# Kernel tuning notes

Measured on AMD Instinct MI355X. Metric: run time of the kernel, lower is better.

Reference implementation:

```python
import jax, jax.numpy as jnp
import numpy as np

N_NODES = 100000
N_EDGES = 3200000
D_IN = 128
D_HID = 128
D_FF = 256
N_CLASSES = 26
N_GRAPHS = 512


def setup_inputs() -> dict:
    key = jax.random.key(0)
    ks = jax.random.split(key, 12)
    s = 0.05
    return {
        "x": jax.random.normal(ks[0], (N_NODES, D_IN), dtype=jnp.float32),
        "edge_index": jax.random.randint(ks[1], (2, N_EDGES), 0, N_NODES, dtype=jnp.int64),
        "batch": jnp.sort(jax.random.randint(ks[2], (N_NODES,), 0, N_GRAPHS, dtype=jnp.int64)),
        "W1": jax.random.normal(ks[3], (D_IN, D_HID), dtype=jnp.float32) * s,
        "b1": jnp.zeros((D_HID,), dtype=jnp.float32),
        "W2": jax.random.normal(ks[4], (D_HID, D_HID), dtype=jnp.float32) * s,
        "b2": jnp.zeros((D_HID,), dtype=jnp.float32),
        "W3": jax.random.normal(ks[5], (D_HID, D_HID), dtype=jnp.float32) * s,
        "b3": jnp.zeros((D_HID,), dtype=jnp.float32),
        "Wfc": jax.random.normal(ks[6], (D_HID, D_FF), dtype=jnp.float32) * s,
        "bfc": jnp.zeros((D_FF,), dtype=jnp.float32),
        "Wfc2": jax.random.normal(ks[7], (D_FF, N_CLASSES), dtype=jnp.float32) * s,
        "bfc2": jnp.zeros((N_CLASSES,), dtype=jnp.float32),
    }


def _gcn_layer(x, src, dst, norm, W, b):
    # GCNConv: h = x @ W; out[dst] += norm_e * h[src]; out += b
    h = x @ W                                   # [N, D]
    msg = h[src] * norm[:, None]                # [E+N, D] gather + scale
    agg = jax.ops.segment_sum(msg, dst, num_segments=N_NODES)
    return agg + b


def reference(x, edge_index, batch, W1, b1, W2, b2, W3, b3, Wfc, bfc, Wfc2, bfc2):
    # add self-loops (PyG GCNConv default) and compute symmetric normalization once
    loop = jnp.arange(N_NODES, dtype=edge_index.dtype)
    src = jnp.concatenate([edge_index[0], loop])
    dst = jnp.concatenate([edge_index[1], loop])
    deg = jax.ops.segment_sum(jnp.ones_like(dst, dtype=x.dtype), dst, num_segments=N_NODES)
    dinv = jnp.where(deg > 0, jax.lax.rsqrt(deg), 0.0)
    norm = dinv[src] * dinv[dst]               # D^{-1/2} A_hat D^{-1/2}

    h = jax.nn.relu(_gcn_layer(x, src, dst, norm, W1, b1))
    h = jax.nn.relu(_gcn_layer(h, src, dst, norm, W2, b2))
    h = jax.nn.relu(_gcn_layer(h, src, dst, norm, W3, b3))

    # global mean pool over graphs
    sums = jax.ops.segment_sum(h, batch, num_segments=N_GRAPHS)       # [G, D]
    cnts = jax.ops.segment_sum(jnp.ones((h.shape[0],), h.dtype), batch, num_segments=N_GRAPHS)
    pooled = sums / jnp.maximum(cnts, 1.0)[:, None]

    out = jax.nn.relu(pooled @ Wfc + bfc)       # dropout is identity at inference
    return out @ Wfc2 + bfc2                    # [G, num_classes]
```

## Files before the change

### kernel.cpp

```cpp
#include <hip/hip_runtime.h>
#include <hip/hip_bf16.h>

typedef __bf16 bf16;
typedef __attribute__((ext_vector_type(8))) __bf16 bf16x8;
typedef __attribute__((ext_vector_type(4))) __bf16 bf16x4;
typedef __attribute__((ext_vector_type(2))) __bf16 bf16x2;
typedef __attribute__((ext_vector_type(4))) float f32x4;

constexpr int N_NODES   = 100000;
constexpr int N_PAD     = 100032;
constexpr int D         = 128;
constexpr int D_FF      = 256;
constexpr int N_CLASSES = 26;
constexpr int N_GRAPHS  = 512;
constexpr int NB1       = 1024;
constexpr int NBUCK     = (N_NODES + 511) / 512;

__device__ inline float2 bf2f(unsigned u) {
    float lo = __uint_as_float(u << 16);
    float hi = __uint_as_float(u & 0xffff0000u);
    return make_float2(lo, hi);
}


__global__ __launch_bounds__(256) void p1_hist(const int* __restrict__ edst,
                                               int* __restrict__ gcount, int e) {
    __shared__ int cnt[NBUCK];
    for (int t = threadIdx.x; t < NBUCK; t += 256) cnt[t] = 0;
    __syncthreads();
    int chunk = (e + NB1 - 1) / NB1;
    int lo = blockIdx.x * chunk;
    int hi = min(e, lo + chunk);
    for (int i = lo + threadIdx.x; i < hi; i += 256)
        atomicAdd(&cnt[edst[i] >> 9], 1);
    __syncthreads();
    for (int t = threadIdx.x; t < NBUCK; t += 256)
        gcount[t * NB1 + blockIdx.x] = cnt[t];
}

__global__ __launch_bounds__(256) void scan1(const int* __restrict__ in,
                                             int* out, int* bsum, int n) {
    __shared__ int sd[256];
    int i = blockIdx.x * 256 + threadIdx.x;
    int v = (i < n) ? in[i] : 0;
    sd[threadIdx.x] = v; __syncthreads();
    for (int off = 1; off < 256; off <<= 1) {
        int t = (threadIdx.x >= off) ? sd[threadIdx.x - off] : 0;
        __syncthreads();
        sd[threadIdx.x] += t;
        __syncthreads();
    }
    if (i < n) out[i + 1] = sd[threadIdx.x];
    if (threadIdx.x == 255) bsum[blockIdx.x] = sd[255];
}

__global__ __launch_bounds__(1024) void scan2(const int* __restrict__ bsum,
                                              int* boff, int nb) {
    __shared__ int sd[1024];
    int t = threadIdx.x;
    int v = (t < nb) ? bsum[t] : 0;
    sd[t] = v; __syncthreads();
    for (int off = 1; off < 1024; off <<= 1) {
        int x = (t >= off) ? sd[t - off] : 0;
        __syncthreads();
        sd[t] += x;
        __syncthreads();
    }
    if (t < nb) boff[t] = sd[t] - v;
}

__global__ void scan3(int* out, const int* __restrict__ boff, int n) {
    int i = blockIdx.x * 256 + threadIdx.x;
    if (i < n) out[i + 1] += boff[blockIdx.x];
    if (i == 0) out[0] = 0;
}

__global__ __launch_bounds__(256) void p3_scatter(const int* __restrict__ esrc,
                                                  const int* __restrict__ edst,
                                                  const int* __restrict__ gbase,
                                                  int* __restrict__ ebuf, int e) {
    __shared__ int cur[NBUCK];
    for (int t = threadIdx.x; t < NBUCK; t += 256)
        cur[t] = gbase[t * NB1 + blockIdx.x];
    __syncthreads();
    int chunk = (e + NB1 - 1) / NB1;
    int lo = blockIdx.x * chunk;
    int hi = min(e, lo + chunk);
    for (int i = lo + threadIdx.x; i < hi; i += 256) {
        int d = edst[i], s = esrc[i];
        int pos = atomicAdd(&cur[d >> 9], 1);
        ebuf[pos] = (s << 9) | (d & 511);
    }
}

__global__ __launch_bounds__(256) void p45_fill(const int* __restrict__ ebuf,
                                                const int* __restrict__ gbase,
                                                float* __restrict__ dinv,
                                                int* __restrict__ rowptr,
                                                int* __restrict__ csrc, int e, int n) {
    __shared__ int cnt[512];
    __shared__ int ps[256];
    __shared__ int cur[512];
    int b = blockIdx.x, t = threadIdx.x;
    cnt[t] = 0; cnt[t + 256] = 0;
    __syncthreads();
    int lo = gbase[b * NB1];
    int hi = (b + 1 < NBUCK) ? gbase[(b + 1) * NB1] : e;
    for (int i = lo + t; i < hi; i += 256)
        atomicAdd(&cnt[ebuf[i] & 511], 1);
    __syncthreads();
    int a0 = cnt[t * 2], a1 = cnt[t * 2 + 1];
    ps[t] = a0 + a1;
    __syncthreads();
    for (int off = 1; off < 256; off <<= 1) {
        int v = (t >= off) ? ps[t - off] : 0;
        __syncthreads();
        ps[t] += v;
        __syncthreads();
    }
    int pexcl = (t > 0) ? ps[t - 1] : 0;
    int g0 = lo + pexcl;
    int node0 = b * 512 + t * 2;
    cur[t * 2] = g0;
    cur[t * 2 + 1] = g0 + a0;
    if (node0 < n) {
        rowptr[node0] = g0;
        dinv[node0] = 1.0f / sqrtf((float)(a0 + 1));
    }
    if (node0 + 1 < n) {
        rowptr[node0 + 1] = g0 + a0;
        dinv[node0 + 1] = 1.0f / sqrtf((float)(a1 + 1));
    }
    if (b == 0 && t == 0) rowptr[n] = e;
    __syncthreads();
    for (int i = lo + t; i < hi; i += 256) {
        int pe = ebuf[i];
        int pos = atomicAdd(&cur[pe & 511], 1);
        csrc[pos] = pe >> 9;
    }
}

__global__ __launch_bounds__(576) void starts_kernel(const int* __restrict__ batch,
                                                     int* __restrict__ starts, int n) {
    int g = threadIdx.x;
    if (g > N_GRAPHS) return;
    int lo = 0, hi = n;
    while (lo < hi) {
        int mid = (lo + hi) >> 1;
        if (batch[mid] < g) lo = mid + 1; else hi = mid;
    }
    starts[g] = lo;
}


__global__ void castWT3_kernel(const float* __restrict__ W0,
                               const float* __restrict__ W1,
                               const float* __restrict__ W2,
                               bf16* __restrict__ WT3) {
    int n = blockIdx.x, l = blockIdx.y, k = threadIdx.x;
    const float* W = (l == 0) ? W0 : (l == 1) ? W1 : W2;
    WT3[l * D * D + n * D + k] = (bf16)W[k * D + n];
}

__global__ __launch_bounds__(256) void gemm_kernel(const bf16* __restrict__ A,
                                                   const bf16* __restrict__ WT,
                                                   bf16* __restrict__ C) {
    int wave = threadIdx.x >> 6;
    int lane = threadIdx.x & 63;
    int m16  = lane & 15;
    int quad = lane >> 4;
    int row0 = blockIdx.x * 64 + wave * 16;

    bf16x8 a[4];
    const bf16* arow = A + (row0 + m16) * D + quad * 8;
#pragma unroll
    for (int kt = 0; kt < 4; ++kt)
        a[kt] = *(const bf16x8*)(arow + kt * 32);

#pragma unroll
    for (int nt = 0; nt < 8; ++nt) {
        f32x4 acc = {0.f, 0.f, 0.f, 0.f};
        const bf16* brow = WT + (nt * 16 + m16) * D + quad * 8;
#pragma unroll
        for (int kt = 0; kt < 4; ++kt) {
            bf16x8 b = *(const bf16x8*)(brow + kt * 32);
            acc = __builtin_amdgcn_mfma_f32_16x16x32_bf16(a[kt], b, acc, 0, 0, 0);
        }
#pragma unroll
        for (int r = 0; r < 4; ++r)
            C[(row0 + quad * 4 + r) * D + nt * 16 + m16] = (bf16)acc[r];
    }
}

__global__ __launch_bounds__(256) void gemm_f32_kernel(const float* __restrict__ A,
                                                       const bf16* __restrict__ WT,
                                                       bf16* __restrict__ C, int n) {
    int wave = threadIdx.x >> 6;
    int lane = threadIdx.x & 63;
    int m16  = lane & 15;
    int quad = lane >> 4;
    int row0 = blockIdx.x * 64 + wave * 16;
    int arowi = row0 + m16;

    bf16x8 a[4];
    const float* arow = A + (size_t)arowi * D + quad * 8;
#pragma unroll
    for (int kt = 0; kt < 4; ++kt) {
        float4 f0 = make_float4(0.f, 0.f, 0.f, 0.f);
        float4 f1 = make_float4(0.f, 0.f, 0.f, 0.f);
        if (arowi < n) {
            f0 = *(const float4*)(arow + kt * 32);
            f1 = *(const float4*)(arow + kt * 32 + 4);
        }
        bf16x8 v = { (bf16)f0.x, (bf16)f0.y, (bf16)f0.z, (bf16)f0.w,
                     (bf16)f1.x, (bf16)f1.y, (bf16)f1.z, (bf16)f1.w };
        a[kt] = v;
    }

#pragma unroll
    for (int nt = 0; nt < 8; ++nt) {
        f32x4 acc = {0.f, 0.f, 0.f, 0.f};
        const bf16* brow = WT + (nt * 16 + m16) * D + quad * 8;
#pragma unroll
        for (int kt = 0; kt < 4; ++kt) {
            bf16x8 b = *(const bf16x8*)(brow + kt * 32);
            acc = __builtin_amdgcn_mfma_f32_16x16x32_bf16(a[kt], b, acc, 0, 0, 0);
        }
#pragma unroll
        for (int r = 0; r < 4; ++r)
            C[(row0 + quad * 4 + r) * D + nt * 16 + m16] = (bf16)acc[r];
    }
}

__global__ __launch_bounds__(256) void spmm_kernel(const bf16* __restrict__ h,
                                                   const int* __restrict__ rowptr,
                                                   const int* __restrict__ csrc,
                                                   const float* __restrict__ dinv,
                                                   const float* __restrict__ bias,
                                                   bf16* __restrict__ out, int n) {
    int v = blockIdx.x * 4 + (threadIdx.x >> 6);
    if (v >= n) return;
    int lane = threadIdx.x & 63;
    int g = lane >> 4;
    int c = lane & 15;
    int s = rowptr[v], e = rowptr[v + 1];
    float dv = dinv[v];

    float acc[8] = {0.f, 0.f, 0.f, 0.f, 0.f, 0.f, 0.f, 0.f};

    if (g == 0) {
        uint4 u = *(const uint4*)(h + v * D + c * 8);
        float s2 = dv * dv;
        float2 f0 = bf2f(u.x), f1 = bf2f(u.y), f2 = bf2f(u.z), f3 = bf2f(u.w);
        acc[0] = s2 * f0.x; acc[1] = s2 * f0.y;
        acc[2] = s2 * f1.x; acc[3] = s2 * f1.y;
        acc[4] = s2 * f2.x; acc[5] = s2 * f2.y;
        acc[6] = s2 * f3.x; acc[7] = s2 * f3.y;
    }

    int j = s + g;
    for (; j + 4 < e; j += 8) {
        int s0 = csrc[j], s1 = csrc[j + 4];
        float w0 = dinv[s0] * dv, w1 = dinv[s1] * dv;
        uint4 ua = *(const uint4*)(h + s0 * D + c * 8);
        uint4 ub = *(const uint4*)(h + s1 * D + c * 8);
        float2 a0 = bf2f(ua.x), a1 = bf2f(ua.y), a2 = bf2f(ua.z), a3 = bf2f(ua.w);
        float2 b0 = bf2f(ub.x), b1 = bf2f(ub.y), b2 = bf2f(ub.z), b3 = bf2f(ub.w);
        acc[0] = fmaf(w0, a0.x, acc[0]); acc[1] = fmaf(w0, a0.y, acc[1]);
        acc[2] = fmaf(w0, a1.x, acc[2]); acc[3] = fmaf(w0, a1.y, acc[3]);
        acc[4] = fmaf(w0, a2.x, acc[4]); acc[5] = fmaf(w0, a2.y, acc[5]);
        acc[6] = fmaf(w0, a3.x, acc[6]); acc[7] = fmaf(w0, a3.y, acc[7]);
        acc[0] = fmaf(w1, b0.x, acc[0]); acc[1] = fmaf(w1, b0.y, acc[1]);
        acc[2] = fmaf(w1, b1.x, acc[2]); acc[3] = fmaf(w1, b1.y, acc[3]);
        acc[4] = fmaf(w1, b2.x, acc[4]); acc[5] = fmaf(w1, b2.y, acc[5]);
        acc[6] = fmaf(w1, b3.x, acc[6]); acc[7] = fmaf(w1, b3.y, acc[7]);
    }
    if (j < e) {
        int s0 = csrc[j];
        float w0 = dinv[s0] * dv;
        uint4 ua = *(const uint4*)(h + s0 * D + c * 8);
        float2 a0 = bf2f(ua.x), a1 = bf2f(ua.y), a2 = bf2f(ua.z), a3 = bf2f(ua.w);
        acc[0] = fmaf(w0, a0.x, acc[0]); acc[1] = fmaf(w0, a0.y, acc[1]);
        acc[2] = fmaf(w0, a1.x, acc[2]); acc[3] = fmaf(w0, a1.y, acc[3]);
        acc[4] = fmaf(w0, a2.x, acc[4]); acc[5] = fmaf(w0, a2.y, acc[5]);
        acc[6] = fmaf(w0, a3.x, acc[6]); acc[7] = fmaf(w0, a3.y, acc[7]);
    }

#pragma unroll
    for (int d = 0; d < 8; ++d) {
        acc[d] += __shfl_xor(acc[d], 16);
        acc[d] += __shfl_xor(acc[d], 32);
    }

    if (g == 0) {
        float4 bi0 = *(const float4*)(bias + c * 8);
        float4 bi1 = *(const float4*)(bias + c * 8 + 4);
        bf16x8 o;
        o[0] = (bf16)fmaxf(acc[0] + bi0.x, 0.f);
        o[1] = (bf16)fmaxf(acc[1] + bi0.y, 0.f);
        o[2] = (bf16)fmaxf(acc[2] + bi0.z, 0.f);
        o[3] = (bf16)fmaxf(acc[3] + bi0.w, 0.f);
        o[4] = (bf16)fmaxf(acc[4] + bi1.x, 0.f);
        o[5] = (bf16)fmaxf(acc[5] + bi1.y, 0.f);
        o[6] = (bf16)fmaxf(acc[6] + bi1.z, 0.f);
        o[7] = (bf16)fmaxf(acc[7] + bi1.w, 0.f);
        *(bf16x8*)(out + v * D + c * 8) = o;
    }
}

__global__ __launch_bounds__(256) void pool_kernel(const bf16* __restrict__ h,
                                                   const int* __restrict__ starts,
                                                   float* __restrict__ pooled) {
    __shared__ float part[3][D];
    int g = blockIdx.x;
    int w = threadIdx.x >> 6, lane = threadIdx.x & 63;
    int s = starts[g], e = starts[g + 1];
    float ax = 0.f, ay = 0.f;
    for (int r = s + w; r < e; r += 4) {
        unsigned u = *(const unsigned*)(h + r * D + lane * 2);
        float2 f = bf2f(u);
        ax += f.x; ay += f.y;
    }
    if (w > 0) { part[w - 1][lane * 2] = ax; part[w - 1][lane * 2 + 1] = ay; }
    __syncthreads();
    if (w == 0) {
#pragma unroll
        for (int k = 0; k < 3; ++k) { ax += part[k][lane * 2]; ay += part[k][lane * 2 + 1]; }
        float c = fmaxf((float)(e - s), 1.0f);
        pooled[g * D + lane * 2]     = ax / c;
        pooled[g * D + lane * 2 + 1] = ay / c;
    }
}

__global__ __launch_bounds__(256) void fc_kernel(const float* __restrict__ pooled,
                                                 const float* __restrict__ Wfc,
                                                 const float* __restrict__ bfc,
                                                 const float* __restrict__ Wfc2,
                                                 const float* __restrict__ bfc2,
                                                 float* __restrict__ out) {
    __shared__ float pr[D];
    __shared__ float hid[D_FF];
    int g = blockIdx.x, t = threadIdx.x;
    if (t < D) pr[t] = pooled[g * D + t];
    __syncthreads();
    float acc = bfc[t];
    for (int k = 0; k < D; ++k) acc = fmaf(pr[k], Wfc[k * D_FF + t], acc);
    hid[t] = fmaxf(acc, 0.f);
    __syncthreads();
    if (t < N_CLASSES) {
        float o = bfc2[t];
        for (int k = 0; k < D_FF; ++k) o = fmaf(hid[k], Wfc2[k * N_CLASSES + t], o);
        out[g * N_CLASSES + t] = o;
    }
}


extern "C" void kernel_launch(void* const* d_in, const int* in_sizes, int n_in,
                              void* d_out, int out_size, void* d_ws, size_t ws_size,
                              hipStream_t stream) {
    const float* x     = (const float*)d_in[0];
    const int*   eidx  = (const int*)d_in[1];
    const int*   batch = (const int*)d_in[2];
    const float* W[3]  = { (const float*)d_in[3], (const float*)d_in[5], (const float*)d_in[7] };
    const float* b[3]  = { (const float*)d_in[4], (const float*)d_in[6], (const float*)d_in[8] };
    const float* Wfc   = (const float*)d_in[9];
    const float* bfc   = (const float*)d_in[10];
    const float* Wfc2  = (const float*)d_in[11];
    const float* bfc2  = (const float*)d_in[12];
    float* out = (float*)d_out;

    const int E = in_sizes[1] / 2;
    const int N = in_sizes[0] / D;
    const int* esrc = eidx;
    const int* edst = eidx + E;

    uint8_t* base = (uint8_t*)d_ws;
    size_t off = 0;
    auto alloc = [&](size_t bytes) -> void* {
        void* p = base + off;
        off = (off + bytes + 255) & ~(size_t)255;
        return p;
    };
    bf16*  hA     = (bf16*) alloc((size_t)N_PAD * D * 2);
    bf16*  hB     = (bf16*) alloc((size_t)N_PAD * D * 2);
    bf16*  WT3    = (bf16*) alloc((size_t)3 * D * D * 2);
    int*   csrc   = (int*)  alloc((size_t)E * 4);
    int*   ebuf   = (int*)  alloc((size_t)E * 4);
    int*   gcount = (int*)  alloc((size_t)NBUCK * NB1 * 4);
    int*   gbase  = (int*)  alloc((size_t)(NBUCK * NB1 + 1) * 4);
    int*   rowptr = (int*)  alloc((size_t)(N + 1) * 4);
    float* dinv   = (float*)alloc((size_t)N * 4);
    int*   bsum   = (int*)  alloc(4096);
    int*   boff   = (int*)  alloc(4096);
    int*   starts = (int*)  alloc((size_t)(N_GRAPHS + 1) * 4);
    float* pooled = (float*)alloc((size_t)N_GRAPHS * D * 4);
    (void)ws_size; (void)n_in; (void)out_size;

    const int GB  = N_PAD / 64;
    const int SB  = (N + 3) / 4;
    const int GCN = NBUCK * NB1;
    const int GCB = (GCN + 255) / 256;

    p1_hist<<<NB1, 256, 0, stream>>>(edst, gcount, E);
    scan1<<<GCB, 256, 0, stream>>>(gcount, gbase, bsum, GCN);
    scan2<<<1, 1024, 0, stream>>>(bsum, boff, GCB);
    scan3<<<GCB, 256, 0, stream>>>(gbase, boff, GCN);
    p3_scatter<<<NB1, 256, 0, stream>>>(esrc, edst, gbase, ebuf, E);
    p45_fill<<<NBUCK, 256, 0, stream>>>(ebuf, gbase, dinv, rowptr, csrc, E, N);

    starts_kernel<<<1, 576, 0, stream>>>(batch, starts, N);

    castWT3_kernel<<<dim3(D, 3), D, 0, stream>>>(W[0], W[1], W[2], WT3);

    gemm_f32_kernel<<<GB, 256, 0, stream>>>(x, WT3, hA, N);
    spmm_kernel<<<SB, 256, 0, stream>>>(hA, rowptr, csrc, dinv, b[0], hB, N);
    for (int l = 1; l < 3; ++l) {
        gemm_kernel<<<GB, 256, 0, stream>>>(hB, WT3 + (size_t)l * D * D, hA);
        spmm_kernel<<<SB, 256, 0, stream>>>(hA, rowptr, csrc, dinv, b[l], hB, N);
    }

    pool_kernel<<<N_GRAPHS, 256, 0, stream>>>(hB, starts, pooled);
    fc_kernel<<<N_GRAPHS, 256, 0, stream>>>(pooled, Wfc, bfc, Wfc2, bfc2, out);
}
```

Baseline: 675.2 us.

## Fuse preprocessing kernels, single-block scan, and merge pooling with FC head

Merges the first-layer GEMM, the edge-destination histogram and the graph-start search into one multi-role prep kernel. The three-pass scan becomes a single-block scan, and the histogram block count drops from 1024 to 256. Scatter and fill kernels move to 512 threads, and pooling is fused with the MLP head. The aim is to cut kernel launches and shrink the scan. The cost is less parallelism in the histogram and scatter stages, plus a serial per-thread scan loop.

New measurement: 719.2 us. 1.07x slower.

```diff
diff --git a/kernel.cpp b/kernel.cpp
--- a/kernel.cpp
+++ b/kernel.cpp
@@ -3,8 +3,6 @@
 
 typedef __bf16 bf16;
 typedef __attribute__((ext_vector_type(8))) __bf16 bf16x8;
-typedef __attribute__((ext_vector_type(4))) __bf16 bf16x4;
-typedef __attribute__((ext_vector_type(2))) __bf16 bf16x2;
 typedef __attribute__((ext_vector_type(4))) float f32x4;
 
 constexpr int N_NODES   = 100000;
@@ -13,8 +11,10 @@
 constexpr int D_FF      = 256;
 constexpr int N_CLASSES = 26;
 constexpr int N_GRAPHS  = 512;
-constexpr int NB1       = 1024;
+constexpr int NB1       = 256;
 constexpr int NBUCK     = (N_NODES + 511) / 512;
+constexpr int GB        = N_PAD / 64;
+constexpr int GCN       = NBUCK * NB1;
 
 __device__ inline float2 bf2f(unsigned u) {
     float lo = __uint_as_float(u << 16);
@@ -22,136 +22,152 @@
     return make_float2(lo, hi);
 }
 
-
-__global__ __launch_bounds__(256) void p1_hist(const int* __restrict__ edst,
-                                               int* __restrict__ gcount, int e) {
+__global__ __launch_bounds__(256) void prep_kernel(const float* __restrict__ x,
+                                                   const bf16* __restrict__ WT,
+                                                   bf16* __restrict__ hA,
+                                                   const int* __restrict__ edst,
+                                                   int* __restrict__ gcount,
+                                                   const int* __restrict__ batch,
+                                                   int* __restrict__ starts,
+                                                   int e, int n) {
     __shared__ int cnt[NBUCK];
-    for (int t = threadIdx.x; t < NBUCK; t += 256) cnt[t] = 0;
-    __syncthreads();
-    int chunk = (e + NB1 - 1) / NB1;
-    int lo = blockIdx.x * chunk;
-    int hi = min(e, lo + chunk);
-    for (int i = lo + threadIdx.x; i < hi; i += 256)
-        atomicAdd(&cnt[edst[i] >> 9], 1);
-    __syncthreads();
-    for (int t = threadIdx.x; t < NBUCK; t += 256)
-        gcount[t * NB1 + blockIdx.x] = cnt[t];
-}
-
-__global__ __launch_bounds__(256) void scan1(const int* __restrict__ in,
-                                             int* out, int* bsum, int n) {
-    __shared__ int sd[256];
-    int i = blockIdx.x * 256 + threadIdx.x;
-    int v = (i < n) ? in[i] : 0;
-    sd[threadIdx.x] = v; __syncthreads();
-    for (int off = 1; off < 256; off <<= 1) {
-        int t = (threadIdx.x >= off) ? sd[threadIdx.x - off] : 0;
-        __syncthreads();
-        sd[threadIdx.x] += t;
-        __syncthreads();
-    }
-    if (i < n) out[i + 1] = sd[threadIdx.x];
-    if (threadIdx.x == 255) bsum[blockIdx.x] = sd[255];
-}
-
-__global__ __launch_bounds__(1024) void scan2(const int* __restrict__ bsum,
-                                              int* boff, int nb) {
+    int bx = blockIdx.x;
+    if (bx < GB) {
+        int wave = threadIdx.x >> 6;
+        int lane = threadIdx.x & 63;
+        int m16  = lane & 15;
+        int quad = lane >> 4;
+        int row0 = bx * 64 + wave * 16;
+        int arowi = row0 + m16;
+
+        bf16x8 a[4];
+        const float* arow = x + (size_t)arowi * D + quad * 8;
+#pragma unroll
+        for (int kt = 0; kt < 4; ++kt) {
+            float4 f0 = make_float4(0.f, 0.f, 0.f, 0.f);
+            float4 f1 = make_float4(0.f, 0.f, 0.f, 0.f);
+            if (arowi < n) {
+                f0 = *(const float4*)(arow + kt * 32);
+                f1 = *(const float4*)(arow + kt * 32 + 4);
+            }
+            bf16x8 v = { (bf16)f0.x, (bf16)f0.y, (bf16)f0.z, (bf16)f0.w,
+                         (bf16)f1.x, (bf16)f1.y, (bf16)f1.z, (bf16)f1.w };
+            a[kt] = v;
+        }
+#pragma unroll
+        for (int nt = 0; nt < 8; ++nt) {
+            f32x4 acc = {0.f, 0.f, 0.f, 0.f};
+            const bf16* brow = WT + (nt * 16 + m16) * D + quad * 8;
+#pragma unroll
+            for (int kt = 0; kt < 4; ++kt) {
+                bf16x8 b = *(const bf16x8*)(brow + kt * 32);
+                acc = __builtin_amdgcn_mfma_f32_16x16x32_bf16(a[kt], b, acc, 0, 0, 0);
+            }
+#pragma unroll
+            for (int r = 0; r < 4; ++r)
+                hA[(row0 + quad * 4 + r) * D + nt * 16 + m16] = (bf16)acc[r];
+        }
+    } else if (bx < GB + NB1) {
+        int b = bx - GB;
+        for (int t = threadIdx.x; t < NBUCK; t += 256) cnt[t] = 0;
+        __syncthreads();
+        int chunk = (e + NB1 - 1) / NB1;
+        int lo = b * chunk;
+        int hi = min(e, lo + chunk);
+        for (int i = lo + threadIdx.x; i < hi; i += 256)
+            atomicAdd(&cnt[edst[i] >> 9], 1);
+        __syncthreads();
+        for (int t = threadIdx.x; t < NBUCK; t += 256)
+            gcount[t * NB1 + b] = cnt[t];
+    } else {
+        for (int g = threadIdx.x; g <= N_GRAPHS; g += 256) {
+            int lo = 0, hi = n;
+            while (lo < hi) {
+                int mid = (lo + hi) >> 1;
+                if (batch[mid] < g) lo = mid + 1; else hi = mid;
+            }
+            starts[g] = lo;
+        }
+    }
+}
+
+__global__ __launch_bounds__(1024) void scan_single(const int* __restrict__ in,
+                                                    int* __restrict__ outx, int n) {
     __shared__ int sd[1024];
     int t = threadIdx.x;
-    int v = (t < nb) ? bsum[t] : 0;
-    sd[t] = v; __syncthreads();
+    const int CH = (n + 1023) / 1024;
+    int lo = t * CH, hi = min(n, lo + CH);
+    int sum = 0;
+    for (int i = lo; i < hi; ++i) sum += in[i];
+    sd[t] = sum; __syncthreads();
     for (int off = 1; off < 1024; off <<= 1) {
-        int x = (t >= off) ? sd[t - off] : 0;
-        __syncthreads();
-        sd[t] += x;
-        __syncthreads();
-    }
-    if (t < nb) boff[t] = sd[t] - v;
-}
-
-__global__ void scan3(int* out, const int* __restrict__ boff, int n) {
-    int i = blockIdx.x * 256 + threadIdx.x;
-    if (i < n) out[i + 1] += boff[blockIdx.x];
-    if (i == 0) out[0] = 0;
-}
-
-__global__ __launch_bounds__(256) void p3_scatter(const int* __restrict__ esrc,
+        int v = (t >= off) ? sd[t - off] : 0;
+        __syncthreads();
+        sd[t] += v;
+        __syncthreads();
+    }
+    int run = sd[t] - sum;
+    for (int i = lo; i < hi; ++i) { int v = in[i]; outx[i] = run; run += v; }
+}
+
+__global__ __launch_bounds__(512) void p3_scatter(const int* __restrict__ esrc,
                                                   const int* __restrict__ edst,
                                                   const int* __restrict__ gbase,
                                                   int* __restrict__ ebuf, int e) {
     __shared__ int cur[NBUCK];
-    for (int t = threadIdx.x; t < NBUCK; t += 256)
+    for (int t = threadIdx.x; t < NBUCK; t += 512)
         cur[t] = gbase[t * NB1 + blockIdx.x];
     __syncthreads();
     int chunk = (e + NB1 - 1) / NB1;
     int lo = blockIdx.x * chunk;
     int hi = min(e, lo + chunk);
-    for (int i = lo + threadIdx.x; i < hi; i += 256) {
+    for (int i = lo + threadIdx.x; i < hi; i += 512) {
         int d = edst[i], s = esrc[i];
         int pos = atomicAdd(&cur[d >> 9], 1);
         ebuf[pos] = (s << 9) | (d & 511);
     }
 }
 
-__global__ __launch_bounds__(256) void p45_fill(const int* __restrict__ ebuf,
+__global__ __launch_bounds__(512) void p45_fill(const int* __restrict__ ebuf,
                                                 const int* __restrict__ gbase,
                                                 float* __restrict__ dinv,
                                                 int* __restrict__ rowptr,
                                                 int* __restrict__ csrc, int e, int n) {
     __shared__ int cnt[512];
-    __shared__ int ps[256];
+    __shared__ int ps[512];
     __shared__ int cur[512];
     int b = blockIdx.x, t = threadIdx.x;
-    cnt[t] = 0; cnt[t + 256] = 0;
+    cnt[t] = 0;
     __syncthreads();
     int lo = gbase[b * NB1];
     int hi = (b + 1 < NBUCK) ? gbase[(b + 1) * NB1] : e;
-    for (int i = lo + t; i < hi; i += 256)
+    for (int i = lo + t; i < hi; i += 512)
         atomicAdd(&cnt[ebuf[i] & 511], 1);
     __syncthreads();
-    int a0 = cnt[t * 2], a1 = cnt[t * 2 + 1];
-    ps[t] = a0 + a1;
-    __syncthreads();
-    for (int off = 1; off < 256; off <<= 1) {
+    int a = cnt[t];
+    ps[t] = a;
+    __syncthreads();
+    for (int off = 1; off < 512; off <<= 1) {
         int v = (t >= off) ? ps[t - off] : 0;
         __syncthreads();
         ps[t] += v;
         __syncthreads();
     }
-    int pexcl = (t > 0) ? ps[t - 1] : 0;
-    int g0 = lo + pexcl;
-    int node0 = b * 512 + t * 2;
-    cur[t * 2] = g0;
-    cur[t * 2 + 1] = g0 + a0;
-    if (node0 < n) {
-        rowptr[node0] = g0;
-        dinv[node0] = 1.0f / sqrtf((float)(a0 + 1));
-    }
-    if (node0 + 1 < n) {
-        rowptr[node0 + 1] = g0 + a0;
-        dinv[node0 + 1] = 1.0f / sqrtf((float)(a1 + 1));
+    int g0 = lo + ps[t] - a;
+    int node = b * 512 + t;
+    cur[t] = g0;
+    if (node < n) {
+        rowptr[node] = g0;
+        dinv[node] = 1.0f / sqrtf((float)(a + 1));
     }
     if (b == 0 && t == 0) rowptr[n] = e;
     __syncthreads();
-    for (int i = lo + t; i < hi; i += 256) {
+    for (int i = lo + t; i < hi; i += 512) {
         int pe = ebuf[i];
         int pos = atomicAdd(&cur[pe & 511], 1);
         csrc[pos] = pe >> 9;
     }
 }
-
-__global__ __launch_bounds__(576) void starts_kernel(const int* __restrict__ batch,
-                                                     int* __restrict__ starts, int n) {
-    int g = threadIdx.x;
-    if (g > N_GRAPHS) return;
-    int lo = 0, hi = n;
-    while (lo < hi) {
-        int mid = (lo + hi) >> 1;
-        if (batch[mid] < g) lo = mid + 1; else hi = mid;
-    }
-    starts[g] = lo;
-}
-
 
 __global__ void castWT3_kernel(const float* __restrict__ W0,
                                const float* __restrict__ W1,
@@ -176,46 +192,6 @@
 #pragma unroll
     for (int kt = 0; kt < 4; ++kt)
         a[kt] = *(const bf16x8*)(arow + kt * 32);
-
-#pragma unroll
-    for (int nt = 0; nt < 8; ++nt) {
-        f32x4 acc = {0.f, 0.f, 0.f, 0.f};
-        const bf16* brow = WT + (nt * 16 + m16) * D + quad * 8;
-#pragma unroll
-        for (int kt = 0; kt < 4; ++kt) {
-            bf16x8 b = *(const bf16x8*)(brow + kt * 32);
-            acc = __builtin_amdgcn_mfma_f32_16x16x32_bf16(a[kt], b, acc, 0, 0, 0);
-        }
-#pragma unroll
-        for (int r = 0; r < 4; ++r)
-            C[(row0 + quad * 4 + r) * D + nt * 16 + m16] = (bf16)acc[r];
-    }
-}
-
-__global__ __launch_bounds__(256) void gemm_f32_kernel(const float* __restrict__ A,
-                                                       const bf16* __restrict__ WT,
-                                                       bf16* __restrict__ C, int n) {
-    int wave = threadIdx.x >> 6;
-    int lane = threadIdx.x & 63;
-    int m16  = lane & 15;
-    int quad = lane >> 4;
-    int row0 = blockIdx.x * 64 + wave * 16;
-    int arowi = row0 + m16;
-
-    bf16x8 a[4];
-    const float* arow = A + (size_t)arowi * D + quad * 8;
-#pragma unroll
-    for (int kt = 0; kt < 4; ++kt) {
-        float4 f0 = make_float4(0.f, 0.f, 0.f, 0.f);
-        float4 f1 = make_float4(0.f, 0.f, 0.f, 0.f);
-        if (arowi < n) {
-            f0 = *(const float4*)(arow + kt * 32);
-            f1 = *(const float4*)(arow + kt * 32 + 4);
-        }
-        bf16x8 v = { (bf16)f0.x, (bf16)f0.y, (bf16)f0.z, (bf16)f0.w,
-                     (bf16)f1.x, (bf16)f1.y, (bf16)f1.z, (bf16)f1.w };
-        a[kt] = v;
-    }
 
 #pragma unroll
     for (int nt = 0; nt < 8; ++nt) {
@@ -308,10 +284,16 @@
     }
 }
 
-__global__ __launch_bounds__(256) void pool_kernel(const bf16* __restrict__ h,
-                                                   const int* __restrict__ starts,
-                                                   float* __restrict__ pooled) {
+__global__ __launch_bounds__(256) void poolfc_kernel(const bf16* __restrict__ h,
+                                                     const int* __restrict__ starts,
+                                                     const float* __restrict__ Wfc,
+                                                     const float* __restrict__ bfc,
+                                                     const float* __restrict__ Wfc2,
+                                                     const float* __restrict__ bfc2,
+                                                     float* __restrict__ out) {
     __shared__ float part[3][D];
+    __shared__ float pr[D];
+    __shared__ float hid[D_FF];
     int g = blockIdx.x;
     int w = threadIdx.x >> 6, lane = threadIdx.x & 63;
     int s = starts[g], e = starts[g + 1];
@@ -327,22 +309,11 @@
 #pragma unroll
         for (int k = 0; k < 3; ++k) { ax += part[k][lane * 2]; ay += part[k][lane * 2 + 1]; }
         float c = fmaxf((float)(e - s), 1.0f);
-        pooled[g * D + lane * 2]     = ax / c;
-        pooled[g * D + lane * 2 + 1] = ay / c;
-    }
-}
-
-__global__ __launch_bounds__(256) void fc_kernel(const float* __restrict__ pooled,
-                                                 const float* __restrict__ Wfc,
-                                                 const float* __restrict__ bfc,
-                                                 const float* __restrict__ Wfc2,
-                                                 const float* __restrict__ bfc2,
-                                                 float* __restrict__ out) {
-    __shared__ float pr[D];
-    __shared__ float hid[D_FF];
-    int g = blockIdx.x, t = threadIdx.x;
-    if (t < D) pr[t] = pooled[g * D + t];
-    __syncthreads();
+        pr[lane * 2]     = ax / c;
+        pr[lane * 2 + 1] = ay / c;
+    }
+    __syncthreads();
+    int t = threadIdx.x;
     float acc = bfc[t];
     for (int k = 0; k < D; ++k) acc = fmaf(pr[k], Wfc[k * D_FF + t], acc);
     hid[t] = fmaxf(acc, 0.f);
@@ -386,39 +357,29 @@
     bf16*  WT3    = (bf16*) alloc((size_t)3 * D * D * 2);
     int*   csrc   = (int*)  alloc((size_t)E * 4);
     int*   ebuf   = (int*)  alloc((size_t)E * 4);
-    int*   gcount = (int*)  alloc((size_t)NBUCK * NB1 * 4);
-    int*   gbase  = (int*)  alloc((size_t)(NBUCK * NB1 + 1) * 4);
+    int*   gcount = (int*)  alloc((size_t)GCN * 4);
+    int*   gbase  = (int*)  alloc((size_t)(GCN + 1) * 4);
     int*   rowptr = (int*)  alloc((size_t)(N + 1) * 4);
     float* dinv   = (float*)alloc((size_t)N * 4);
-    int*   bsum   = (int*)  alloc(4096);
-    int*   boff   = (int*)  alloc(4096);
     int*   starts = (int*)  alloc((size_t)(N_GRAPHS + 1) * 4);
-    float* pooled = (float*)alloc((size_t)N_GRAPHS * D * 4);
     (void)ws_size; (void)n_in; (void)out_size;
 
-    const int GB  = N_PAD / 64;
-    const int SB  = (N + 3) / 4;
-    const int GCN = NBUCK * NB1;
-    const int GCB = (GCN + 255) / 256;
-
-    p1_hist<<<NB1, 256, 0, stream>>>(edst, gcount, E);
-    scan1<<<GCB, 256, 0, stream>>>(gcount, gbase, bsum, GCN);
-    scan2<<<1, 1024, 0, stream>>>(bsum, boff, GCB);
-    scan3<<<GCB, 256, 0, stream>>>(gbase, boff, GCN);
-    p3_scatter<<<NB1, 256, 0, stream>>>(esrc, edst, gbase, ebuf, E);
-    p45_fill<<<NBUCK, 256, 0, stream>>>(ebuf, gbase, dinv, rowptr, csrc, E, N);
-
-    starts_kernel<<<1, 576, 0, stream>>>(batch, starts, N);
+    const int SB = (N + 3) / 4;
 
     castWT3_kernel<<<dim3(D, 3), D, 0, stream>>>(W[0], W[1], W[2], WT3);
 
-    gemm_f32_kernel<<<GB, 256, 0, stream>>>(x, WT3, hA, N);
+    prep_kernel<<<GB + NB1 + 1, 256, 0, stream>>>(x, WT3, hA, edst, gcount,
+                                                  batch, starts, E, N);
+
+    scan_single<<<1, 1024, 0, stream>>>(gcount, gbase, GCN);
+    p3_scatter<<<NB1, 512, 0, stream>>>(esrc, edst, gbase, ebuf, E);
+    p45_fill<<<NBUCK, 512, 0, stream>>>(ebuf, gbase, dinv, rowptr, csrc, E, N);
+
     spmm_kernel<<<SB, 256, 0, stream>>>(hA, rowptr, csrc, dinv, b[0], hB, N);
     for (int l = 1; l < 3; ++l) {
         gemm_kernel<<<GB, 256, 0, stream>>>(hB, WT3 + (size_t)l * D * D, hA);
         spmm_kernel<<<SB, 256, 0, stream>>>(hA, rowptr, csrc, dinv, b[l], hB, N);
     }
 
-    pool_kernel<<<N_GRAPHS, 256, 0, stream>>>(hB, starts, pooled);
-    fc_kernel<<<N_GRAPHS, 256, 0, stream>>>(pooled, Wfc, bfc, Wfc2, bfc2, out);
-}
+    poolfc_kernel<<<N_GRAPHS, 256, 0, stream>>>(hB, starts, Wfc, bfc, Wfc2, bfc2, out);
+}
```
